# Kernel optimization log

Measured on AMD Instinct MI355X. Metric: run time of the kernel, lower is better.

The kernel has to match this reference:

```python
import jax, jax.numpy as jnp
import numpy as np

EPS = 1e-7        # keras backend epsilon
ALPHA = 0.25
GAMMA = 2.0
NEG_INF = -1e30

B, T, V, L = 256, 1024, 128, 64
BLANK = V - 1     # blank_index=-1 in tf ctc_loss_v2


def setup_inputs() -> dict:
    key = jax.random.key(0)
    k1, k2 = jax.random.split(key)
    y_pred = jax.random.uniform(k1, (B, T, V), dtype=jnp.float32)
    y_true = jax.random.randint(k2, (B, L), 0, V - 1, dtype=jnp.int32)
    return {"y_true": y_true, "y_pred": y_pred}


def _ctc_neg_log_lik(y_true, y_pred):
    """Standard CTC forward (alpha) DP in log space; full lengths T and L."""
    b, t, v = y_pred.shape
    l = y_true.shape[1]
    s = 2 * l + 1
    # tf ctc_loss_v2 log-softmaxes its logits; logits here are log(y_pred+eps)
    logp = jax.nn.log_softmax(jnp.log(y_pred + EPS), axis=-1)     # [B,T,V]
    # extended label sequence: blank, l1, blank, l2, ..., blank    [B,S]
    ext = jnp.full((b, s), BLANK, dtype=y_true.dtype)
    ext = ext.at[:, 1::2].set(y_true)
    # per-timestep log-probs of extended labels -> [T,B,S]
    lp_ext = jnp.take_along_axis(logp, ext[:, None, :], axis=2)   # [B,T,S]
    lp_ext = jnp.transpose(lp_ext, (1, 0, 2))                     # [T,B,S]
    # skip transition s-2 -> s allowed iff ext[s] != blank and ext[s] != ext[s-2]
    ext_sm2 = jnp.pad(ext[:, :-2], ((0, 0), (2, 0)), constant_values=BLANK)
    allow_skip = (ext != BLANK) & (ext != ext_sm2)                # [B,S]

    alpha0 = jnp.full((b, s), NEG_INF, dtype=logp.dtype)
    alpha0 = alpha0.at[:, 0].set(lp_ext[0, :, 0])
    alpha0 = alpha0.at[:, 1].set(lp_ext[0, :, 1])

    def step(alpha, lp_t):
        a0 = alpha
        a1 = jnp.pad(alpha[:, :-1], ((0, 0), (1, 0)), constant_values=NEG_INF)
        a2 = jnp.pad(alpha[:, :-2], ((0, 0), (2, 0)), constant_values=NEG_INF)
        a2 = jnp.where(allow_skip, a2, NEG_INF)
        m = jnp.maximum(jnp.maximum(a0, a1), a2)                  # stable LSE
        lse = m + jnp.log(jnp.exp(a0 - m) + jnp.exp(a1 - m) + jnp.exp(a2 - m))
        return lse + lp_t, None

    alphaT, _ = jax.lax.scan(step, alpha0, lp_ext[1:])
    log_lik = jnp.logaddexp(alphaT[:, -1], alphaT[:, -2])         # [B]
    return -log_lik


def reference(y_true, y_pred):
    loss = _ctc_neg_log_lik(y_true, y_pred)                       # [B]
    p = jnp.exp(-loss)
    focal = ALPHA * (1.0 - p) ** GAMMA * loss
    return jnp.mean(focal)
```

## Files before the change

### kernel.cpp

```cpp
#include <hip/hip_runtime.h>


#define EPSF 1e-7f

constexpr int Bb = 256;
constexpr int Tt = 1024;
constexpr int Vv = 128;
constexpr int Ll = 64;

template <int Ctrl, int RowMask, int BankMask, bool BoundCtrl>
__device__ __forceinline__ float dppf(float x) {
    return __int_as_float(__builtin_amdgcn_update_dpp(
        0, __float_as_int(x), Ctrl, RowMask, BankMask, BoundCtrl));
}

__device__ __forceinline__ float wave_sum63(float x) {
    x += dppf<0x111, 0xf, 0xf, true>(x);
    x += dppf<0x112, 0xf, 0xf, true>(x);
    x += dppf<0x114, 0xf, 0xf, true>(x);
    x += dppf<0x118, 0xf, 0xf, true>(x);
    x += dppf<0x142, 0xa, 0xf, false>(x);
    x += dppf<0x143, 0xc, 0xf, false>(x);
    return x;
}

__device__ __forceinline__ float half_sum(float x) {
    x += dppf<0x111, 0xf, 0xf, true>(x);
    x += dppf<0x112, 0xf, 0xf, true>(x);
    x += dppf<0x114, 0xf, 0xf, true>(x);
    x += dppf<0x118, 0xf, 0xf, true>(x);
    x += dppf<0x142, 0xa, 0xf, false>(x);
    return x;
}

__device__ __forceinline__ float wave_max63(float x) {
    x = fmaxf(x, dppf<0x111, 0xf, 0xf, true>(x));
    x = fmaxf(x, dppf<0x112, 0xf, 0xf, true>(x));
    x = fmaxf(x, dppf<0x114, 0xf, 0xf, true>(x));
    x = fmaxf(x, dppf<0x118, 0xf, 0xf, true>(x));
    x = fmaxf(x, dppf<0x142, 0xa, 0xf, false>(x));
    x = fmaxf(x, dppf<0x143, 0xc, 0xf, false>(x));
    return x;
}

__device__ __forceinline__ float bcast63(float x) {
    return __int_as_float(__builtin_amdgcn_readlane(__float_as_int(x), 63));
}

__launch_bounds__(1024, 1)
__global__ void fused_kernel(const int* __restrict__ y_true,
                             const float* __restrict__ y_pred,
                             float* __restrict__ focal_ws) {
    const int b    = blockIdx.x;
    const int lane = threadIdx.x & 63;
    const int wv   = threadIdx.x >> 6;

    const float* yb = y_pred + (size_t)b * Tt * Vv;

    __shared__ float part[30];

    float a_odd = 0.0f, a128 = 0.0f;
    int   eacc  = 0;

    if (wv == 0) {
        const int lab  = y_true[b * Ll + lane];
        const int labp = __shfl_up(lab, 1);
        const float maskf = (lane == 0 || lab != labp) ? 1.0f : 0.0f;

        constexpr int PD = 16;
        float bg[PD];
        float bq[PD];
#pragma unroll
        for (int d = 0; d < PD; ++d) {
            bg[d] = yb[d * Vv + lab];
            bq[d] = yb[d * Vv + 127];
        }

        float a_even = (lane == 0) ? 1.0f : 0.0f;

        auto step = [&](float g, float qbl, bool check) {
            const float qe = g + EPSF;
            const float qb = qbl + EPSF;
            const float am1 = dppf<0x138, 0xf, 0xf, true>(a_odd);
            const float ne   = (a_even + am1) * qb;
            const float no   = (a_odd + a_even + maskf * am1) * qe;
            const float n128 = (a128 + a_odd) * qb;
            a_even = ne;
            a_odd  = no;
            a128   = n128;
            if (check) {
                const float m = fmaxf(fmaxf(a_even, a_odd), a128);
                if (__all(m < 0x1p-25f)) {
                    float mm = wave_max63(m);
                    const float    wmax  = bcast63(mm);
                    const unsigned e     = __float_as_uint(wmax) >> 23;
                    const float    scale = __uint_as_float((254u - e) << 23);
                    eacc += (int)e - 127;
                    a_even *= scale;
                    a_odd  *= scale;
                    a128   *= scale;
                }
            }
        };

        for (int tb = 0; tb < Tt - PD; tb += PD) {
#pragma unroll
            for (int j = 0; j < PD; ++j) {
                const float g  = bg[j];
                const float q  = bq[j];
                const int   tn = tb + j + PD;
                bg[j] = yb[tn * Vv + lab];
                bq[j] = yb[tn * Vv + 127];
                step(g, q, (j & 3) == 3);
            }
        }
#pragma unroll
        for (int j = 0; j < PD; ++j) step(bg[j], bq[j], (j & 3) == 3);
    } else {
        const float4* b4 = (const float4*)yb;
        const int w  = wv - 1;
        const int rs = (w * 512) / 15;
        const int re = ((w + 1) * 512) / 15;

        float ll = 0.0f;
        int rp = rs;
        for (; rp + 2 <= re; rp += 2) {
            const float4 v0 = b4[rp * 64 + lane];
            const float4 v1 = b4[rp * 64 + 64 + lane];
            const float s0 = half_sum(v0.x + v0.y + v0.z + v0.w);
            const float s1 = half_sum(v1.x + v1.y + v1.z + v1.w);
            ll += __log2f(s0 + (float)Vv * EPSF) +
                  __log2f(s1 + (float)Vv * EPSF);
        }
        if (rp < re) {
            const float4 v0 = b4[rp * 64 + lane];
            const float s0 = half_sum(v0.x + v0.y + v0.z + v0.w);
            ll += __log2f(s0 + (float)Vv * EPSF);
        }
        if ((lane & 31) == 31) part[2 * w + (lane >> 5)] = ll;
    }

    __syncthreads();

    if (wv == 0) {
        float v = (lane < 30) ? part[lane] : 0.0f;
        v = wave_sum63(v);
        if (lane == 63) {
            const float acc_ld = v;
            const float tot    = fmaxf(a128 + a_odd, 1e-37f);
            const float log2lik = __log2f(tot) + (float)eacc - acc_ld;
            const float ln_lik  = 0.69314718055994530942f * log2lik;
            const float loss    = -ln_lik;
            const float p       = __expf(ln_lik);
            const float om      = 1.0f - p;
            focal_ws[b] = 0.25f * om * om * loss;
        }
    }
}

__global__ void finalize_kernel(const float* __restrict__ focal_ws,
                                float* __restrict__ out) {
    const int i    = threadIdx.x;
    const int lane = i & 63;
    const int wv   = i >> 6;

    float f = focal_ws[i];
#pragma unroll
    for (int off = 32; off > 0; off >>= 1) f += __shfl_xor(f, off);

    __shared__ float red[4];
    if (lane == 0) red[wv] = f;
    __syncthreads();
    if (i == 0)
        out[0] = (red[0] + red[1] + red[2] + red[3]) * (1.0f / (float)Bb);
}

extern "C" void kernel_launch(void* const* d_in, const int* in_sizes, int n_in,
                              void* d_out, int out_size, void* d_ws, size_t ws_size,
                              hipStream_t stream) {
    const int*   y_true = (const int*)d_in[0];
    const float* y_pred = (const float*)d_in[1];
    float* focal_ws = (float*)d_ws;

    fused_kernel<<<Bb, 1024, 0, stream>>>(y_true, y_pred, focal_ws);
    finalize_kernel<<<1, 256, 0, stream>>>(focal_ws, (float*)d_out);
}
```

Measured before the change: 233.2 us.

## Stage y_pred chunks through shared memory so the DP wave reads LDS

Before, wave 0 ran the CTC recurrence by gathering from global memory while 15 other waves computed log-sum normalizers on their own. Now the 15 waves stream 128-timestep chunks of y_pred into a double-buffered LDS tile (64KB+) and compute the normalizers as they go. Wave 0 runs the DP on the previous chunk from LDS, with block-wide syncs between chunks. This swaps high-latency strided global gathers on the serial critical path for LDS reads, at the cost of nine __syncthreads and a large LDS footprint.

Result: faster. 202.3 us (-13.3%).

```diff
diff --git a/kernel.cpp b/kernel.cpp
--- a/kernel.cpp
+++ b/kernel.cpp
@@ -3,10 +3,13 @@
 
 #define EPSF 1e-7f
 
-constexpr int Bb = 256;
-constexpr int Tt = 1024;
-constexpr int Vv = 128;
-constexpr int Ll = 64;
+constexpr int Bb  = 256;
+constexpr int Tt  = 1024;
+constexpr int Vv  = 128;
+constexpr int Ll  = 64;
+constexpr int CH  = 128;
+constexpr int NCH = Tt / CH;
+constexpr int PAIRS = CH / 2;
 
 template <int Ctrl, int RowMask, int BankMask, bool BoundCtrl>
 __device__ __forceinline__ float dppf(float x) {
@@ -55,104 +58,124 @@
     const int lane = threadIdx.x & 63;
     const int wv   = threadIdx.x >> 6;
 
-    const float* yb = y_pred + (size_t)b * Tt * Vv;
-
-    __shared__ float part[30];
-
-    float a_odd = 0.0f, a128 = 0.0f;
-    int   eacc  = 0;
+    const float*  yb  = y_pred + (size_t)b * Tt * Vv;
+    const float4* yb4 = (const float4*)yb;
+
+    __shared__ float4 l4buf[2 * CH * (Vv / 4)];
+    __shared__ float  lblk[2 * CH];
+    __shared__ float  part[30];
+    float* lrows = (float*)l4buf;
+
+    float a_even = 0.0f, a_odd = 0.0f, a128 = 0.0f;
+    int   eacc = 0;
+    float maskf = 0.0f;
+    int   lab = 0;
+
+    const int w    = wv - 1;
+    const int half = lane >> 5;
+    float ll = 0.0f;
 
     if (wv == 0) {
-        const int lab  = y_true[b * Ll + lane];
+        lab = y_true[b * Ll + lane];
         const int labp = __shfl_up(lab, 1);
-        const float maskf = (lane == 0 || lab != labp) ? 1.0f : 0.0f;
-
-        constexpr int PD = 16;
-        float bg[PD];
-        float bq[PD];
-#pragma unroll
-        for (int d = 0; d < PD; ++d) {
-            bg[d] = yb[d * Vv + lab];
-            bq[d] = yb[d * Vv + 127];
+        maskf  = (lane == 0 || lab != labp) ? 1.0f : 0.0f;
+        a_even = (lane == 0) ? 1.0f : 0.0f;
+    }
+
+    auto step = [&](float g, float qbl, bool check) {
+        const float qe  = g + EPSF;
+        const float qb  = qbl + EPSF;
+        const float am1 = dppf<0x138, 0xf, 0xf, true>(a_odd);
+        const float ne   = (a_even + am1) * qb;
+        const float no   = (a_odd + a_even + maskf * am1) * qe;
+        const float n128 = (a128 + a_odd) * qb;
+        a_even = ne;
+        a_odd  = no;
+        a128   = n128;
+        if (check) {
+            const float m = fmaxf(fmaxf(a_even, a_odd), a128);
+            if (__all(m < 0x1p-25f)) {
+                float mm = wave_max63(m);
+                const float    wmax  = bcast63(mm);
+                const unsigned e     = __float_as_uint(wmax) >> 23;
+                const float    scale = __uint_as_float((254u - e) << 23);
+                eacc += (int)e - 127;
+                a_even *= scale;
+                a_odd  *= scale;
+                a128   *= scale;
+            }
         }
-
-        float a_even = (lane == 0) ? 1.0f : 0.0f;
-
-        auto step = [&](float g, float qbl, bool check) {
-            const float qe = g + EPSF;
-            const float qb = qbl + EPSF;
-            const float am1 = dppf<0x138, 0xf, 0xf, true>(a_odd);
-            const float ne   = (a_even + am1) * qb;
-            const float no   = (a_odd + a_even + maskf * am1) * qe;
-            const float n128 = (a128 + a_odd) * qb;
-            a_even = ne;
-            a_odd  = no;
-            a128   = n128;
-            if (check) {
-                const float m = fmaxf(fmaxf(a_even, a_odd), a128);
-                if (__all(m < 0x1p-25f)) {
-                    float mm = wave_max63(m);
-                    const float    wmax  = bcast63(mm);
-                    const unsigned e     = __float_as_uint(wmax) >> 23;
-                    const float    scale = __uint_as_float((254u - e) << 23);
-                    eacc += (int)e - 127;
-                    a_even *= scale;
-                    a_odd  *= scale;
-                    a128   *= scale;
+    };
+
+    for (int p = 0; p <= NCH; ++p) {
+        if (wv != 0) {
+            if (p < NCH) {
+                const int bsel  = p & 1;
+                const int gbase = p * CH * (Vv / 4);
+                const int lbase = bsel * CH * (Vv / 4);
+                float4 v[5];
+                int    rpc[5];
+#pragma unroll
+                for (int k = 0; k < 5; ++k) {
+                    const int rp = w + 15 * k;
+                    rpc[k] = rp < PAIRS ? rp : PAIRS - 1;
+                    v[k]   = yb4[gbase + rpc[k] * 64 + lane];
                 }
-            }
-        };
-
-        for (int tb = 0; tb < Tt - PD; tb += PD) {
-#pragma unroll
-            for (int j = 0; j < PD; ++j) {
-                const float g  = bg[j];
-                const float q  = bq[j];
-                const int   tn = tb + j + PD;
-                bg[j] = yb[tn * Vv + lab];
-                bq[j] = yb[tn * Vv + 127];
-                step(g, q, (j & 3) == 3);
-            }
+#pragma unroll
+                for (int k = 0; k < 5; ++k) {
+                    const bool valid = (w + 15 * k) < PAIRS;
+                    if (valid) {
+                        l4buf[lbase + rpc[k] * 64 + lane] = v[k];
+                        const float s =
+                            half_sum(v[k].x + v[k].y + v[k].z + v[k].w);
+                        if ((lane & 31) == 31) {
+                            lblk[bsel * CH + 2 * rpc[k] + half] = v[k].w;
+                            ll += __log2f(s + (float)Vv * EPSF);
+                        }
+                    }
+                }
+            } else if ((lane & 31) == 31) {
+                part[2 * w + half] = ll;
+            }
+        } else if (p > 0) {
+            const int bsel = (p - 1) & 1;
+            const int cb   = bsel * CH * Vv;
+            const int bb   = bsel * CH;
+            constexpr int PD = 8;
+            float gq[PD], bq[PD];
+#pragma unroll
+            for (int d = 0; d < PD; ++d) {
+                gq[d] = lrows[cb + d * Vv + lab];
+                bq[d] = lblk[bb + d];
+            }
+            for (int t0 = 0; t0 < CH - PD; t0 += PD) {
+#pragma unroll
+                for (int j = 0; j < PD; ++j) {
+                    const float g = gq[j];
+                    const float q = bq[j];
+                    const int  tn = t0 + j + PD;
+                    gq[j] = lrows[cb + tn * Vv + lab];
+                    bq[j] = lblk[bb + tn];
+                    step(g, q, (j & 3) == 3);
+                }
+            }
+#pragma unroll
+            for (int j = 0; j < PD; ++j) step(gq[j], bq[j], (j & 3) == 3);
         }
-#pragma unroll
-        for (int j = 0; j < PD; ++j) step(bg[j], bq[j], (j & 3) == 3);
-    } else {
-        const float4* b4 = (const float4*)yb;
-        const int w  = wv - 1;
-        const int rs = (w * 512) / 15;
-        const int re = ((w + 1) * 512) / 15;
-
-        float ll = 0.0f;
-        int rp = rs;
-        for (; rp + 2 <= re; rp += 2) {
-            const float4 v0 = b4[rp * 64 + lane];
-            const float4 v1 = b4[rp * 64 + 64 + lane];
-            const float s0 = half_sum(v0.x + v0.y + v0.z + v0.w);
-            const float s1 = half_sum(v1.x + v1.y + v1.z + v1.w);
-            ll += __log2f(s0 + (float)Vv * EPSF) +
-                  __log2f(s1 + (float)Vv * EPSF);
-        }
-        if (rp < re) {
-            const float4 v0 = b4[rp * 64 + lane];
-            const float s0 = half_sum(v0.x + v0.y + v0.z + v0.w);
-            ll += __log2f(s0 + (float)Vv * EPSF);
-        }
-        if ((lane & 31) == 31) part[2 * w + (lane >> 5)] = ll;
+        __syncthreads();
     }
 
-    __syncthreads();
-
     if (wv == 0) {
-        float v = (lane < 30) ? part[lane] : 0.0f;
-        v = wave_sum63(v);
+        float vs = (lane < 30) ? part[lane] : 0.0f;
+        vs = wave_sum63(vs);
         if (lane == 63) {
-            const float acc_ld = v;
+            const float acc_ld = vs;
             const float tot    = fmaxf(a128 + a_odd, 1e-37f);
             const float log2lik = __log2f(tot) + (float)eacc - acc_ld;
             const float ln_lik  = 0.69314718055994530942f * log2lik;
             const float loss    = -ln_lik;
-            const float p       = __expf(ln_lik);
-            const float om      = 1.0f - p;
+            const float pp      = __expf(ln_lik);
+            const float om      = 1.0f - pp;
             focal_ws[b] = 0.25f * om * om * loss;
         }
     }
```
